# Kernel optimization log

Measured on AMD Instinct MI355X. Metric: run time of the kernel, lower is better.

The kernel has to match this reference:

```python
import jax, jax.numpy as jnp
import numpy as np

# Standard FP4 E2M1 lookup table (nvfp4-style): sign bit in nibble MSB.
FP4_LUT = jnp.array([0.0, 0.5, 1.0, 1.5, 2.0, 3.0, 4.0, 6.0,
                     -0.0, -0.5, -1.0, -1.5, -2.0, -3.0, -4.0, -6.0],
                    dtype=jnp.float32)


def dequant_fp4(packed_i32, scales, group_size):
    """packed_i32: [K/8, N] int32 (8 fp4 nibbles per word, low nibble first);
    scales: [K/group_size, N]. Returns dense fp32 weight [K, N]."""
    w = jax.lax.bitcast_convert_type(packed_i32, jnp.uint32)  # [K/8, N]
    # Unpack nibbles along the reduction axis: nibble i -> row 8*r + i.
    nib = jnp.stack([(w >> jnp.uint32(4 * i)) & jnp.uint32(0xF) for i in range(8)],
                    axis=1)                                    # [K/8, 8, N]
    K = nib.shape[0] * 8
    nib = nib.reshape(K, w.shape[1])                           # [K, N]
    vals = FP4_LUT[nib]                                        # [K, N]
    s = jnp.repeat(scales, group_size, axis=0)                 # [K, N]
    return vals * s


def setup_inputs() -> dict:
    key = jax.random.key(0)
    k1, k2, k3, k4, k5, k6 = jax.random.split(key, 6)
    tokens, H, I, G = 4096, 2048, 5632, 128
    return {
        "hidden": jax.random.normal(k1, (tokens, H), dtype=jnp.float32),
        "moe_output": jax.random.normal(k2, (tokens, H), dtype=jnp.float32),
        "gate_up_weights": jax.random.randint(k3, (H // 8, 2 * I), 0, 2147483647, dtype=jnp.int32),
        "gate_up_scales": jax.random.uniform(k4, (H // G, 2 * I), dtype=jnp.float32, minval=0.01, maxval=0.1),
        "down_weights": jax.random.randint(k5, (I // 8, H), 0, 2147483647, dtype=jnp.int32),
        "down_scales": jax.random.uniform(k6, (I // G, H), dtype=jnp.float32, minval=0.01, maxval=0.1),
        "group_size": G,
    }


def reference(hidden, moe_output, gate_up_weights, gate_up_scales,
              down_weights, down_scales, group_size):
    # Shared-expert SwiGLU FFN with FP4 group-quantized weights, fused residual add.
    W_gu = dequant_fp4(gate_up_weights, gate_up_scales, group_size)  # [H, 2I]
    gu = hidden @ W_gu                                               # [T, 2I]
    I = gu.shape[1] // 2
    gate, up = gu[:, :I], gu[:, I:]
    act = jax.nn.silu(gate) * up                                     # [T, I]
    W_d = dequant_fp4(down_weights, down_scales, group_size)         # [I, H]
    return moe_output + act @ W_d                                    # [T, H]
```

## Files before the change

### kernel.cpp

```cpp
#include <hip/hip_runtime.h>
#include <hip/hip_fp16.h>
#include <stdint.h>

#define TOKENS 4096
#define HDIM   2048
#define IDIM   5632
#define BM 128
#define BN 128
#define BK 64

#define G1_NP  11264
#define G1_KSB (G1_NP * 64)

typedef _Float16 f16x8 __attribute__((ext_vector_type(8)));
typedef float    f32x4 __attribute__((ext_vector_type(4)));

__device__ __forceinline__ uint32_t dec2(uint32_t z, uint32_t s2u) {
    uint32_t sgn = (z << 12) & 0x80008000u;
    uint32_t h   = ((z << 9) & 0x0E000E00u) | sgn;
    __half2 hv = __builtin_bit_cast(__half2, h);
    __half2 sv = __builtin_bit_cast(__half2, s2u);
    __half2 r  = __hmul2(hv, sv);
    return __builtin_bit_cast(uint32_t, r);
}
__device__ __forceinline__ int4 dec8(uint32_t w, uint32_t s2u) {
    int4 d;
    d.x = (int)dec2( w        & 0x000F000Fu, s2u);
    d.y = (int)dec2((w >> 4)  & 0x000F000Fu, s2u);
    d.z = (int)dec2((w >> 8)  & 0x000F000Fu, s2u);
    d.w = (int)dec2((w >> 12) & 0x000F000Fu, s2u);
    return d;
}
__device__ __forceinline__ uint32_t scale_s2u(float sc) {
    uint16_t hs = __builtin_bit_cast(uint16_t, __float2half(sc * 16384.0f));
    return (uint32_t)hs * 0x00010001u;
}
__device__ __forceinline__ uint32_t packh(float lo, float hi) {
    __half2 h2 = __halves2half2(__float2half(lo), __float2half(hi));
    return __builtin_bit_cast(uint32_t, h2);
}
__device__ __forceinline__ void gl_lds16(const void* g, void* l) {
    __builtin_amdgcn_global_load_lds(
        (const __attribute__((address_space(1))) uint32_t*)g,
        (__attribute__((address_space(3))) uint32_t*)l, 16, 0, 0);
}

__global__ __launch_bounds__(256) void convert_hidden(
    const float* __restrict__ src, __half* __restrict__ dst)
{
    int idx = blockIdx.x * 256 + threadIdx.x;
    const float4* s = (const float4*)src + (size_t)idx * 2;
    float4 a = s[0], b = s[1];
    int4 v;
    v.x = (int)packh(a.x, b.x);
    v.y = (int)packh(a.y, b.y);
    v.z = (int)packh(a.z, b.z);
    v.w = (int)packh(a.w, b.w);
    *((int4*)dst + idx) = v;
}

__global__ __launch_bounds__(256) void dequant_wgu(
    const uint32_t* __restrict__ W, const float* __restrict__ S,
    __half* __restrict__ Bt)
{
    int kt = blockIdx.y;
    int np = blockIdx.x * 32 + (threadIdx.x >> 3);
    int j  = threadIdx.x & 7;
    int within = np & 15;
    int pair   = np >> 5;
    int sel    = (np >> 4) & 1;
    int sc = pair * 16 + within + (sel ? IDIM : 0);
    uint32_t s2u = scale_s2u(S[(size_t)(kt >> 1) * (2 * IDIM) + sc]);
    uint32_t w   = W[(size_t)(kt * 8 + j) * (2 * IDIM) + sc];
    int4 d = dec8(w, s2u);
    *(int4*)(Bt + (size_t)kt * G1_KSB + (size_t)np * 64 + j * 8) = d;
}

__global__ __launch_bounds__(256, 4) void gemm1_s(
    const __half* __restrict__ A, const __half* __restrict__ Bt,
    __half* __restrict__ act)
{
    __shared__ __half Alds[BM * 64];
    __shared__ __half Blds[BN * 64];
    const int tid  = threadIdx.x;
    const int lane = tid & 63;
    const int wid  = tid >> 6;
    const int wm = wid >> 1, wn = wid & 1;
    const int m0 = blockIdx.y * BM;
    const int n0 = blockIdx.x * BN;

    f32x4 acc[4][4];
    #pragma unroll
    for (int i = 0; i < 4; ++i)
        #pragma unroll
        for (int j = 0; j < 4; ++j) acc[i][j] = f32x4{0.f, 0.f, 0.f, 0.f};

    const __half* srcA[4];
    const __half* srcB[4];
    #pragma unroll
    for (int i = 0; i < 4; ++i) {
        int u = i * 256 + tid, row = u >> 3, s = u & 7, sl = s ^ (row & 7);
        srcA[i] = A  + (size_t)(m0 + row) * HDIM + sl * 8;
        srcB[i] = Bt + (size_t)(n0 + row) * 64 + sl * 8;
    }

    for (int kt = 0; kt < HDIM / 64; ++kt) {
        #pragma unroll
        for (int i = 0; i < 4; ++i) {
            int u = i * 256 + tid;
            gl_lds16(srcA[i] + (size_t)kt * 64,      (char*)Alds + u * 16);
            gl_lds16(srcB[i] + (size_t)kt * G1_KSB,  (char*)Blds + u * 16);
        }
        __syncthreads();
        #pragma unroll
        for (int ks = 0; ks < 2; ++ks) {
            f16x8 af[4], bf[4];
            const int kb = ks * 4 + (lane >> 4);
            #pragma unroll
            for (int mi = 0; mi < 4; ++mi) {
                int r = wm * 64 + mi * 16 + (lane & 15);
                af[mi] = *(const f16x8*)&Alds[r * 64 + ((kb ^ (r & 7)) << 3)];
            }
            #pragma unroll
            for (int ni = 0; ni < 4; ++ni) {
                int r = wn * 64 + ni * 16 + (lane & 15);
                bf[ni] = *(const f16x8*)&Blds[r * 64 + ((kb ^ (r & 7)) << 3)];
            }
            #pragma unroll
            for (int mi = 0; mi < 4; ++mi)
                #pragma unroll
                for (int ni = 0; ni < 4; ++ni)
                    acc[mi][ni] = __builtin_amdgcn_mfma_f32_16x16x32_f16(af[mi], bf[ni], acc[mi][ni], 0, 0, 0);
        }
        __syncthreads();
    }

    #pragma unroll
    for (int mi = 0; mi < 4; ++mi) {
        #pragma unroll
        for (int q = 0; q < 2; ++q) {
            int gc = ((n0 + wn * 64 + q * 32) >> 5) * 16 + (lane & 15);
            int colstore = (gc & ~7) | (((gc & 3) << 1) | ((gc >> 2) & 1));
            #pragma unroll
            for (int r = 0; r < 4; ++r) {
                int m = m0 + wm * 64 + mi * 16 + (lane >> 4) * 4 + r;
                float gv = acc[mi][2 * q][r];
                float uv = acc[mi][2 * q + 1][r];
                float sig = 1.0f / (1.0f + __expf(-gv));
                act[(size_t)m * IDIM + colstore] = __float2half(gv * sig * uv);
            }
        }
    }
}

__global__ __launch_bounds__(256, 2) void gemm1_silu(
    const __half* __restrict__ A, const uint32_t* __restrict__ W,
    const float* __restrict__ S, __half* __restrict__ act)
{
    __shared__ __half Alds[BM * BK];
    __shared__ __half Blds[2][BN * BK];
    const int tid  = threadIdx.x;
    const int lane = tid & 63;
    const int wid  = tid >> 6;
    const int wm = wid >> 1, wn = wid & 1;
    const int m0 = blockIdx.y * BM;
    const int c0 = blockIdx.x * BN;

    f32x4 accg[4][4], accu[4][4];
    #pragma unroll
    for (int i = 0; i < 4; ++i)
        #pragma unroll
        for (int j = 0; j < 4; ++j) {
            accg[i][j] = f32x4{0.f, 0.f, 0.f, 0.f};
            accu[i][j] = f32x4{0.f, 0.f, 0.f, 0.f};
        }

    const int c = tid & 127;
    const int rbase = (tid >> 7) * 4;

    for (int kt = 0; kt < HDIM / BK; ++kt) {
        const int k0 = kt * BK;
        #pragma unroll
        for (int i = 0; i < 4; ++i) {
            int u = tid + i * 256;
            int row = u >> 3, kb = u & 7;
            int4 v = *(const int4*)(A + (size_t)(m0 + row) * HDIM + k0 + kb * 8);
            *(int4*)((char*)Alds + row * 128 + ((kb ^ (row & 7)) << 4)) = v;
        }
        const int g = k0 >> 7;
        #pragma unroll
        for (int p = 0; p < 2; ++p) {
            const int ncol = (p ? IDIM : 0) + c0 + c;
            uint32_t s2u = scale_s2u(S[(size_t)g * (2 * IDIM) + ncol]);
            #pragma unroll
            for (int i = 0; i < 4; ++i) {
                int rl = rbase + i;
                uint32_t w = W[(size_t)(kt * 8 + rl) * (2 * IDIM) + ncol];
                int4 d = dec8(w, s2u);
                *(int4*)((char*)&Blds[p][0] + c * 128 + ((rl ^ (c & 7)) << 4)) = d;
            }
        }
        __syncthreads();
        #pragma unroll
        for (int ks = 0; ks < 2; ++ks) {
            f16x8 af[4], bg[4], bu[4];
            const int kb = ks * 4 + (lane >> 4);
            #pragma unroll
            for (int mi = 0; mi < 4; ++mi) {
                int m = wm * 64 + mi * 16 + (lane & 15);
                af[mi] = *(const f16x8*)((const char*)Alds + m * 128 + ((kb ^ (m & 7)) << 4));
            }
            #pragma unroll
            for (int ni = 0; ni < 4; ++ni) {
                int n = wn * 64 + ni * 16 + (lane & 15);
                bg[ni] = *(const f16x8*)((const char*)&Blds[0][0] + n * 128 + ((kb ^ (n & 7)) << 4));
                bu[ni] = *(const f16x8*)((const char*)&Blds[1][0] + n * 128 + ((kb ^ (n & 7)) << 4));
            }
            #pragma unroll
            for (int mi = 0; mi < 4; ++mi)
                #pragma unroll
                for (int ni = 0; ni < 4; ++ni) {
                    accg[mi][ni] = __builtin_amdgcn_mfma_f32_16x16x32_f16(af[mi], bg[ni], accg[mi][ni], 0, 0, 0);
                    accu[mi][ni] = __builtin_amdgcn_mfma_f32_16x16x32_f16(af[mi], bu[ni], accu[mi][ni], 0, 0, 0);
                }
        }
        __syncthreads();
    }
    #pragma unroll
    for (int mi = 0; mi < 4; ++mi) {
        #pragma unroll
        for (int ni = 0; ni < 4; ++ni) {
            int nlog = c0 + wn * 64 + ni * 16 + (lane & 15);
            int ncol = (nlog & ~7) | (((nlog & 3) << 1) | ((nlog >> 2) & 1));
            #pragma unroll
            for (int r = 0; r < 4; ++r) {
                int m = m0 + wm * 64 + mi * 16 + (lane >> 4) * 4 + r;
                float gv = accg[mi][ni][r];
                float uv = accu[mi][ni][r];
                float sig = 1.0f / (1.0f + __expf(-gv));
                act[(size_t)m * IDIM + ncol] = __float2half(gv * sig * uv);
            }
        }
    }
}

__global__ __launch_bounds__(256, 2) void gemm2_add(
    const __half* __restrict__ A, const uint32_t* __restrict__ W,
    const float* __restrict__ S, const float* __restrict__ moe,
    float* __restrict__ out)
{
    __shared__ __half Alds[BM * BK];
    __shared__ __half Blds[BN * BK];
    const int tid  = threadIdx.x;
    const int lane = tid & 63;
    const int wid  = tid >> 6;
    const int wm = wid >> 1, wn = wid & 1;
    const int m0 = blockIdx.y * BM;
    const int n0 = blockIdx.x * BN;

    f32x4 acc[4][4];
    #pragma unroll
    for (int i = 0; i < 4; ++i)
        #pragma unroll
        for (int j = 0; j < 4; ++j) acc[i][j] = f32x4{0.f, 0.f, 0.f, 0.f};

    const int c = tid & 127;
    const int rbase = (tid >> 7) * 4;

    for (int kt = 0; kt < IDIM / BK; ++kt) {
        const int k0 = kt * BK;
        #pragma unroll
        for (int i = 0; i < 4; ++i) {
            int u = tid + i * 256;
            int row = u >> 3, kb = u & 7;
            int4 v = *(const int4*)(A + (size_t)(m0 + row) * IDIM + k0 + kb * 8);
            *(int4*)((char*)Alds + row * 128 + ((kb ^ (row & 7)) << 4)) = v;
        }
        {
            const int g = k0 >> 7;
            const int ncol = n0 + c;
            uint32_t s2u = scale_s2u(S[(size_t)g * HDIM + ncol]);
            #pragma unroll
            for (int i = 0; i < 4; ++i) {
                int rl = rbase + i;
                uint32_t w = W[(size_t)(kt * 8 + rl) * HDIM + ncol];
                int4 d = dec8(w, s2u);
                *(int4*)((char*)Blds + c * 128 + ((rl ^ (c & 7)) << 4)) = d;
            }
        }
        __syncthreads();
        #pragma unroll
        for (int ks = 0; ks < 2; ++ks) {
            f16x8 af[4], bf[4];
            const int kb = ks * 4 + (lane >> 4);
            #pragma unroll
            for (int mi = 0; mi < 4; ++mi) {
                int m = wm * 64 + mi * 16 + (lane & 15);
                af[mi] = *(const f16x8*)((const char*)Alds + m * 128 + ((kb ^ (m & 7)) << 4));
            }
            #pragma unroll
            for (int ni = 0; ni < 4; ++ni) {
                int n = wn * 64 + ni * 16 + (lane & 15);
                bf[ni] = *(const f16x8*)((const char*)Blds + n * 128 + ((kb ^ (n & 7)) << 4));
            }
            #pragma unroll
            for (int mi = 0; mi < 4; ++mi)
                #pragma unroll
                for (int ni = 0; ni < 4; ++ni)
                    acc[mi][ni] = __builtin_amdgcn_mfma_f32_16x16x32_f16(af[mi], bf[ni], acc[mi][ni], 0, 0, 0);
        }
        __syncthreads();
    }
    #pragma unroll
    for (int mi = 0; mi < 4; ++mi) {
        #pragma unroll
        for (int ni = 0; ni < 4; ++ni) {
            int n = n0 + wn * 64 + ni * 16 + (lane & 15);
            #pragma unroll
            for (int r = 0; r < 4; ++r) {
                int m = m0 + wm * 64 + mi * 16 + (lane >> 4) * 4 + r;
                out[(size_t)m * HDIM + n] = moe[(size_t)m * HDIM + n] + acc[mi][ni][r];
            }
        }
    }
}

extern "C" void kernel_launch(void* const* d_in, const int* in_sizes, int n_in,
                              void* d_out, int out_size, void* d_ws, size_t ws_size,
                              hipStream_t stream) {
    const float*    hidden = (const float*)d_in[0];
    const float*    moe    = (const float*)d_in[1];
    const uint32_t* wgu    = (const uint32_t*)d_in[2];
    const float*    sgu    = (const float*)d_in[3];
    const uint32_t* wd     = (const uint32_t*)d_in[4];
    const float*    sd     = (const float*)d_in[5];
    float* out = (float*)d_out;

    __half* hidden_f16 = (__half*)d_ws;
    __half* act        = (__half*)((char*)d_ws + (size_t)TOKENS * HDIM * 2);
    size_t need = (size_t)TOKENS * HDIM * 2 + (size_t)TOKENS * IDIM * 2
                + (size_t)HDIM * (2 * IDIM) * 2;

    convert_hidden<<<dim3(TOKENS * HDIM / 8 / 256), dim3(256), 0, stream>>>(hidden, hidden_f16);
    if (ws_size >= need) {
        __half* wgu16 = (__half*)((char*)d_ws + (size_t)TOKENS * HDIM * 2
                                              + (size_t)TOKENS * IDIM * 2);
        dequant_wgu<<<dim3(G1_NP / 32, 32), dim3(256), 0, stream>>>(wgu, sgu, wgu16);
        gemm1_s<<<dim3(IDIM * 2 / BN, TOKENS / BM), dim3(256), 0, stream>>>(hidden_f16, wgu16, act);
    } else {
        gemm1_silu<<<dim3(IDIM / BN, TOKENS / BM), dim3(256), 0, stream>>>(hidden_f16, wgu, sgu, act);
    }
    gemm2_add<<<dim3(HDIM / BN, TOKENS / BM), dim3(256), 0, stream>>>(act, wd, sd, moe, out);
}
```

Measured before the change: 328.8 us.

## Pre-dequantize down weights to fp16 and use simple streaming GEMM2

Adds a separate dequant_wd kernel that expands the FP4 down-projection weights into a K-blocked fp16 layout in the workspace. A new gemm2_s kernel then streams A and B tiles straight into LDS, replacing the fused in-loop dequantization in gemm2_add. dequant_wgu is also reworked so each thread decodes all 8 words of one column. This costs an extra pass over the weights and extra workspace, and falls back to the old path when the workspace is too small.

```diff
diff --git a/kernel.cpp b/kernel.cpp
--- a/kernel.cpp
+++ b/kernel.cpp
@@ -11,6 +11,7 @@
 
 #define G1_NP  11264
 #define G1_KSB (G1_NP * 64)
+#define G2_KSB (HDIM * 64)
 
 typedef _Float16 f16x8 __attribute__((ext_vector_type(8)));
 typedef float    f32x4 __attribute__((ext_vector_type(4)));
@@ -64,16 +65,32 @@
     __half* __restrict__ Bt)
 {
     int kt = blockIdx.y;
-    int np = blockIdx.x * 32 + (threadIdx.x >> 3);
-    int j  = threadIdx.x & 7;
-    int within = np & 15;
-    int pair   = np >> 5;
-    int sel    = (np >> 4) & 1;
-    int sc = pair * 16 + within + (sel ? IDIM : 0);
+    int np = blockIdx.x * 256 + threadIdx.x;
+    int sc = (np >> 5) * 16 + (np & 15) + (((np >> 4) & 1) ? IDIM : 0);
     uint32_t s2u = scale_s2u(S[(size_t)(kt >> 1) * (2 * IDIM) + sc]);
-    uint32_t w   = W[(size_t)(kt * 8 + j) * (2 * IDIM) + sc];
-    int4 d = dec8(w, s2u);
-    *(int4*)(Bt + (size_t)kt * G1_KSB + (size_t)np * 64 + j * 8) = d;
+    __half* dst = Bt + (size_t)kt * G1_KSB + (size_t)np * 64;
+    #pragma unroll
+    for (int j = 0; j < 8; ++j) {
+        uint32_t w = W[(size_t)(kt * 8 + j) * (2 * IDIM) + sc];
+        int4 d = dec8(w, s2u);
+        *(int4*)(dst + j * 8) = d;
+    }
+}
+
+__global__ __launch_bounds__(256) void dequant_wd(
+    const uint32_t* __restrict__ W, const float* __restrict__ S,
+    __half* __restrict__ Bt)
+{
+    int kt = blockIdx.y;
+    int n  = blockIdx.x * 256 + threadIdx.x;
+    uint32_t s2u = scale_s2u(S[(size_t)(kt >> 1) * HDIM + n]);
+    __half* dst = Bt + (size_t)kt * G2_KSB + (size_t)n * 64;
+    #pragma unroll
+    for (int j = 0; j < 8; ++j) {
+        uint32_t w = W[(size_t)(kt * 8 + j) * HDIM + n];
+        int4 d = dec8(w, s2u);
+        *(int4*)(dst + j * 8) = d;
+    }
 }
 
 __global__ __launch_bounds__(256, 4) void gemm1_s(
@@ -148,6 +165,78 @@
                 float uv = acc[mi][2 * q + 1][r];
                 float sig = 1.0f / (1.0f + __expf(-gv));
                 act[(size_t)m * IDIM + colstore] = __float2half(gv * sig * uv);
+            }
+        }
+    }
+}
+
+__global__ __launch_bounds__(256, 4) void gemm2_s(
+    const __half* __restrict__ A, const __half* __restrict__ Bt,
+    const float* __restrict__ moe, float* __restrict__ out)
+{
+    __shared__ __half Alds[BM * 64];
+    __shared__ __half Blds[BN * 64];
+    const int tid  = threadIdx.x;
+    const int lane = tid & 63;
+    const int wid  = tid >> 6;
+    const int wm = wid >> 1, wn = wid & 1;
+    const int m0 = blockIdx.y * BM;
+    const int n0 = blockIdx.x * BN;
+
+    f32x4 acc[4][4];
+    #pragma unroll
+    for (int i = 0; i < 4; ++i)
+        #pragma unroll
+        for (int j = 0; j < 4; ++j) acc[i][j] = f32x4{0.f, 0.f, 0.f, 0.f};
+
+    const __half* srcA[4];
+    const __half* srcB[4];
+    #pragma unroll
+    for (int i = 0; i < 4; ++i) {
+        int u = i * 256 + tid, row = u >> 3, s = u & 7, sl = s ^ (row & 7);
+        srcA[i] = A  + (size_t)(m0 + row) * IDIM + sl * 8;
+        srcB[i] = Bt + (size_t)(n0 + row) * 64 + sl * 8;
+    }
+
+    for (int kt = 0; kt < IDIM / 64; ++kt) {
+        #pragma unroll
+        for (int i = 0; i < 4; ++i) {
+            int u = i * 256 + tid;
+            gl_lds16(srcA[i] + (size_t)kt * 64,      (char*)Alds + u * 16);
+            gl_lds16(srcB[i] + (size_t)kt * G2_KSB,  (char*)Blds + u * 16);
+        }
+        __syncthreads();
+        #pragma unroll
+        for (int ks = 0; ks < 2; ++ks) {
+            f16x8 af[4], bf[4];
+            const int kb = ks * 4 + (lane >> 4);
+            #pragma unroll
+            for (int mi = 0; mi < 4; ++mi) {
+                int r = wm * 64 + mi * 16 + (lane & 15);
+                af[mi] = *(const f16x8*)&Alds[r * 64 + ((kb ^ (r & 7)) << 3)];
+            }
+            #pragma unroll
+            for (int ni = 0; ni < 4; ++ni) {
+                int r = wn * 64 + ni * 16 + (lane & 15);
+                bf[ni] = *(const f16x8*)&Blds[r * 64 + ((kb ^ (r & 7)) << 3)];
+            }
+            #pragma unroll
+            for (int mi = 0; mi < 4; ++mi)
+                #pragma unroll
+                for (int ni = 0; ni < 4; ++ni)
+                    acc[mi][ni] = __builtin_amdgcn_mfma_f32_16x16x32_f16(af[mi], bf[ni], acc[mi][ni], 0, 0, 0);
+        }
+        __syncthreads();
+    }
+    #pragma unroll
+    for (int mi = 0; mi < 4; ++mi) {
+        #pragma unroll
+        for (int ni = 0; ni < 4; ++ni) {
+            int n = n0 + wn * 64 + ni * 16 + (lane & 15);
+            #pragma unroll
+            for (int r = 0; r < 4; ++r) {
+                int m = m0 + wm * 64 + mi * 16 + (lane >> 4) * 4 + r;
+                out[(size_t)m * HDIM + n] = moe[(size_t)m * HDIM + n] + acc[mi][ni][r];
             }
         }
     }
@@ -336,19 +425,32 @@
     const float*    sd     = (const float*)d_in[5];
     float* out = (float*)d_out;
 
+    const size_t sz_hidden = (size_t)TOKENS * HDIM * 2;
+    const size_t sz_act    = (size_t)TOKENS * IDIM * 2;
+    const size_t sz_wgu16  = (size_t)HDIM * 2 * IDIM * 2;
+    const size_t sz_wd16   = (size_t)IDIM * HDIM * 2;
+
     __half* hidden_f16 = (__half*)d_ws;
-    __half* act        = (__half*)((char*)d_ws + (size_t)TOKENS * HDIM * 2);
-    size_t need = (size_t)TOKENS * HDIM * 2 + (size_t)TOKENS * IDIM * 2
-                + (size_t)HDIM * (2 * IDIM) * 2;
+    __half* act        = (__half*)((char*)d_ws + sz_hidden);
+    __half* wgu16      = (__half*)((char*)d_ws + sz_hidden + sz_act);
+    __half* wd16       = (__half*)((char*)d_ws + sz_hidden + sz_act + sz_wgu16);
+
+    const size_t need_g1 = sz_hidden + sz_act + sz_wgu16;
+    const size_t need_g2 = need_g1 + sz_wd16;
 
     convert_hidden<<<dim3(TOKENS * HDIM / 8 / 256), dim3(256), 0, stream>>>(hidden, hidden_f16);
-    if (ws_size >= need) {
-        __half* wgu16 = (__half*)((char*)d_ws + (size_t)TOKENS * HDIM * 2
-                                              + (size_t)TOKENS * IDIM * 2);
-        dequant_wgu<<<dim3(G1_NP / 32, 32), dim3(256), 0, stream>>>(wgu, sgu, wgu16);
+
+    if (ws_size >= need_g1) {
+        dequant_wgu<<<dim3(G1_NP / 256, 32), dim3(256), 0, stream>>>(wgu, sgu, wgu16);
         gemm1_s<<<dim3(IDIM * 2 / BN, TOKENS / BM), dim3(256), 0, stream>>>(hidden_f16, wgu16, act);
     } else {
         gemm1_silu<<<dim3(IDIM / BN, TOKENS / BM), dim3(256), 0, stream>>>(hidden_f16, wgu, sgu, act);
     }
-    gemm2_add<<<dim3(HDIM / BN, TOKENS / BM), dim3(256), 0, stream>>>(act, wd, sd, moe, out);
-}
+
+    if (ws_size >= need_g2) {
+        dequant_wd<<<dim3(HDIM / 256, IDIM / 64), dim3(256), 0, stream>>>(wd, sd, wd16);
+        gemm2_s<<<dim3(HDIM / BN, TOKENS / BM), dim3(256), 0, stream>>>(act, wd16, moe, out);
+    } else {
+        gemm2_add<<<dim3(HDIM / BN, TOKENS / BM), dim3(256), 0, stream>>>(act, wd, sd, moe, out);
+    }
+}
```

New measurement: 324.3 us. No clear change (-1.4%).

## Enlarge gemm1 tile to 256x128 with 512 threads and coalesce dequant writes

Applied to the files above, without the earlier changes.

The gate/up GEMM now uses 256x128 output tiles with eight waves per block, so each B tile loaded from the dequantized weight buffer is reused across twice as many rows. This is meant to cut global and LDS traffic per FLOP. The dequant kernel has each thread decode a full 64-element row into swizzled shared memory and then write it out fully coalesced, replacing the previous scattered stores. The cost is more LDS per block (48KB), which may lower occupancy, and an extra shared-memory round trip in dequant.

```diff
diff --git a/kernel.cpp b/kernel.cpp
--- a/kernel.cpp
+++ b/kernel.cpp
@@ -63,31 +63,42 @@
     const uint32_t* __restrict__ W, const float* __restrict__ S,
     __half* __restrict__ Bt)
 {
-    int kt = blockIdx.y;
-    int np = blockIdx.x * 32 + (threadIdx.x >> 3);
-    int j  = threadIdx.x & 7;
-    int within = np & 15;
-    int pair   = np >> 5;
-    int sel    = (np >> 4) & 1;
-    int sc = pair * 16 + within + (sel ? IDIM : 0);
+    __shared__ __half L[256 * 64];
+    const int kt = blockIdx.y;
+    const int t  = threadIdx.x;
+    const int np = blockIdx.x * 256 + t;
+    const int sc = (np >> 5) * 16 + (np & 15) + (((np >> 4) & 1) ? IDIM : 0);
     uint32_t s2u = scale_s2u(S[(size_t)(kt >> 1) * (2 * IDIM) + sc]);
-    uint32_t w   = W[(size_t)(kt * 8 + j) * (2 * IDIM) + sc];
-    int4 d = dec8(w, s2u);
-    *(int4*)(Bt + (size_t)kt * G1_KSB + (size_t)np * 64 + j * 8) = d;
-}
-
-__global__ __launch_bounds__(256, 4) void gemm1_s(
+    #pragma unroll
+    for (int j = 0; j < 8; ++j) {
+        uint32_t w = W[(size_t)(kt * 8 + j) * (2 * IDIM) + sc];
+        int4 d = dec8(w, s2u);
+        *(int4*)&L[t * 64 + ((j ^ (t & 7)) << 3)] = d;
+    }
+    __syncthreads();
+    __half* dst = Bt + (size_t)kt * G1_KSB + (size_t)blockIdx.x * 256 * 64;
+    #pragma unroll
+    for (int k = 0; k < 8; ++k) {
+        int c = k * 256 + t;
+        int row = c >> 3, s = c & 7;
+        int4 d = *(const int4*)&L[row * 64 + ((s ^ (row & 7)) << 3)];
+        *(int4*)(dst + c * 8) = d;
+    }
+}
+
+__global__ __launch_bounds__(512, 4) void gemm1_sx(
     const __half* __restrict__ A, const __half* __restrict__ Bt,
     __half* __restrict__ act)
 {
-    __shared__ __half Alds[BM * 64];
-    __shared__ __half Blds[BN * 64];
+    __shared__ __half Alds[256 * 64];
+    __shared__ __half Blds[128 * 64];
     const int tid  = threadIdx.x;
     const int lane = tid & 63;
     const int wid  = tid >> 6;
-    const int wm = wid >> 1, wn = wid & 1;
-    const int m0 = blockIdx.y * BM;
-    const int n0 = blockIdx.x * BN;
+    const int wm = wid >> 1;
+    const int wn = wid & 1;
+    const int m0 = blockIdx.y * 256;
+    const int n0 = blockIdx.x * 128;
 
     f32x4 acc[4][4];
     #pragma unroll
@@ -96,21 +107,25 @@
         for (int j = 0; j < 4; ++j) acc[i][j] = f32x4{0.f, 0.f, 0.f, 0.f};
 
     const __half* srcA[4];
-    const __half* srcB[4];
+    const __half* srcB[2];
     #pragma unroll
     for (int i = 0; i < 4; ++i) {
-        int u = i * 256 + tid, row = u >> 3, s = u & 7, sl = s ^ (row & 7);
-        srcA[i] = A  + (size_t)(m0 + row) * HDIM + sl * 8;
+        int u = i * 512 + tid, row = u >> 3, s = u & 7, sl = s ^ (row & 7);
+        srcA[i] = A + (size_t)(m0 + row) * HDIM + sl * 8;
+    }
+    #pragma unroll
+    for (int i = 0; i < 2; ++i) {
+        int u = i * 512 + tid, row = u >> 3, s = u & 7, sl = s ^ (row & 7);
         srcB[i] = Bt + (size_t)(n0 + row) * 64 + sl * 8;
     }
 
     for (int kt = 0; kt < HDIM / 64; ++kt) {
         #pragma unroll
-        for (int i = 0; i < 4; ++i) {
-            int u = i * 256 + tid;
-            gl_lds16(srcA[i] + (size_t)kt * 64,      (char*)Alds + u * 16);
-            gl_lds16(srcB[i] + (size_t)kt * G1_KSB,  (char*)Blds + u * 16);
-        }
+        for (int i = 0; i < 4; ++i)
+            gl_lds16(srcA[i] + (size_t)kt * 64, (char*)Alds + (i * 512 + tid) * 16);
+        #pragma unroll
+        for (int i = 0; i < 2; ++i)
+            gl_lds16(srcB[i] + (size_t)kt * G1_KSB, (char*)Blds + (i * 512 + tid) * 16);
         __syncthreads();
         #pragma unroll
         for (int ks = 0; ks < 2; ++ks) {
@@ -336,19 +351,24 @@
     const float*    sd     = (const float*)d_in[5];
     float* out = (float*)d_out;
 
+    const size_t sz_hidden = (size_t)TOKENS * HDIM * 2;
+    const size_t sz_act    = (size_t)TOKENS * IDIM * 2;
+    const size_t sz_wgu16  = (size_t)HDIM * 2 * IDIM * 2;
+
     __half* hidden_f16 = (__half*)d_ws;
-    __half* act        = (__half*)((char*)d_ws + (size_t)TOKENS * HDIM * 2);
-    size_t need = (size_t)TOKENS * HDIM * 2 + (size_t)TOKENS * IDIM * 2
-                + (size_t)HDIM * (2 * IDIM) * 2;
+    __half* act        = (__half*)((char*)d_ws + sz_hidden);
+    __half* wgu16      = (__half*)((char*)d_ws + sz_hidden + sz_act);
+
+    const size_t need_g1 = sz_hidden + sz_act + sz_wgu16;
 
     convert_hidden<<<dim3(TOKENS * HDIM / 8 / 256), dim3(256), 0, stream>>>(hidden, hidden_f16);
-    if (ws_size >= need) {
-        __half* wgu16 = (__half*)((char*)d_ws + (size_t)TOKENS * HDIM * 2
-                                              + (size_t)TOKENS * IDIM * 2);
-        dequant_wgu<<<dim3(G1_NP / 32, 32), dim3(256), 0, stream>>>(wgu, sgu, wgu16);
-        gemm1_s<<<dim3(IDIM * 2 / BN, TOKENS / BM), dim3(256), 0, stream>>>(hidden_f16, wgu16, act);
+
+    if (ws_size >= need_g1) {
+        dequant_wgu<<<dim3(G1_NP / 256, 32), dim3(256), 0, stream>>>(wgu, sgu, wgu16);
+        gemm1_sx<<<dim3(G1_NP / 128, TOKENS / 256), dim3(512), 0, stream>>>(hidden_f16, wgu16, act);
     } else {
         gemm1_silu<<<dim3(IDIM / BN, TOKENS / BM), dim3(256), 0, stream>>>(hidden_f16, wgu, sgu, act);
     }
+
     gemm2_add<<<dim3(HDIM / BN, TOKENS / BM), dim3(256), 0, stream>>>(act, wd, sd, moe, out);
 }
```

Result: no change. 323.1 us (-1.7%).
